# Kernel optimization log

Measured on AMD Instinct MI355X. Metric: run time of the kernel, lower is better.

Reference implementation:

```python
import jax, jax.numpy as jnp
import numpy as np

B, T = 32, 4096
I_CND2 = 512      # 2 * size_i_cnd
EMB = 256         # size_i_embed_ar
H = 896           # size_h_rnn
FC = 896          # size_h_fc
O = 512           # size_o


def setup_inputs() -> dict:
    key = jax.random.key(0)
    ks = jax.random.split(key, 8)
    s = 0.02
    return {
        "reference_sample": jax.random.randint(ks[0], (B, T), 0, O),
        "i_cnd_series": jax.random.normal(ks[1], (B, T, I_CND2), dtype=jnp.float32),
        "emb": jax.random.normal(ks[2], (O, EMB), dtype=jnp.float32) * s,
        "w_ih": jax.random.normal(ks[3], (3 * H, EMB + I_CND2), dtype=jnp.float32) * s,
        "w_hh": jax.random.normal(ks[4], (3 * H, H), dtype=jnp.float32) * s,
        "b_ih": jnp.zeros((3 * H,), jnp.float32),
        "b_hh": jnp.zeros((3 * H,), jnp.float32),
        "fc1_w": jax.random.normal(ks[5], (FC, H), dtype=jnp.float32) * s,
        "fc1_b": jnp.zeros((FC,), jnp.float32),
        "fc2_w": jax.random.normal(ks[6], (O, FC), dtype=jnp.float32) * s,
        "fc2_b": jnp.zeros((O,), jnp.float32),
    }


def _gru_scan(gates_x, w_hh, b_hh):
    # gates_x: (B, T, 3H) precomputed input projections (torch gate order: r, z, n)
    h0 = jnp.zeros((gates_x.shape[0], H), gates_x.dtype)

    def step(h, gx):
        gh = h @ w_hh.T + b_hh
        xr, xz, xn = jnp.split(gx, 3, axis=-1)
        hr, hz, hn = jnp.split(gh, 3, axis=-1)
        r = jax.nn.sigmoid(xr + hr)
        z = jax.nn.sigmoid(xz + hz)
        n = jnp.tanh(xn + r * hn)
        h_new = (1.0 - z) * n + z * h
        return h_new, h_new

    _, hs = jax.lax.scan(step, h0, jnp.swapaxes(gates_x, 0, 1))  # (T, B, H)
    return jnp.swapaxes(hs, 0, 1)  # (B, T, H)


def reference(reference_sample, i_cnd_series, emb, w_ih, w_hh, b_ih, b_hh,
              fc1_w, fc1_b, fc2_w, fc2_b):
    # embedding + concat with conditioning
    x = jnp.concatenate([emb[reference_sample], i_cnd_series], axis=-1)  # (B,T,EMB+2C)
    # batch all input-side GRU matmuls (compute-dense), scan only hidden recurrence
    gates_x = jnp.einsum('btd,gd->btg', x, w_ih) + b_ih  # (B,T,3H)
    o_rnn = _gru_scan(gates_x, w_hh, b_hh)               # (B,T,H)
    hidden = jax.nn.relu(jnp.einsum('bth,fh->btf', o_rnn, fc1_w) + fc1_b)
    return jnp.einsum('btf,of->bto', hidden, fc2_w) + fc2_b  # (B,T,O)
```

## Files before the change

kernel.cpp:

```cpp
#include <hip/hip_runtime.h>

#define B_ 32
#define T_FULL 4096
#define EMB_ 256
#define XD_ 768
#define H_ 896
#define G3_ 2688
#define O_ 512
#define NWG_SCAN 28
#define THR_SCAN 768

typedef __attribute__((ext_vector_type(8))) short bf16x8;
typedef __attribute__((ext_vector_type(4))) float f32x4;
typedef __attribute__((ext_vector_type(16))) float f32x16;

__device__ __forceinline__ f32x4 mfma16(bf16x8 a, bf16x8 b, f32x4 c) {
  return __builtin_amdgcn_mfma_f32_16x16x32_bf16(a, b, c, 0, 0, 0);
}
__device__ __forceinline__ f32x16 mfma32(bf16x8 a, bf16x8 b, f32x16 c) {
  return __builtin_amdgcn_mfma_f32_32x32x16_bf16(a, b, c, 0, 0, 0);
}

__device__ __forceinline__ unsigned short f2bf(float x) {
  union { float f; unsigned u; } v; v.f = x;
  unsigned r = v.u + 0x7fffu + ((v.u >> 16) & 1u);
  return (unsigned short)(r >> 16);
}
__device__ __forceinline__ float bf2f(unsigned short h) {
  union { float f; unsigned u; } v; v.u = ((unsigned)h) << 16;
  return v.f;
}

__device__ __forceinline__ unsigned long long aload64(const unsigned long long* p) {
  return __hip_atomic_load((unsigned long long*)p, __ATOMIC_RELAXED, __HIP_MEMORY_SCOPE_AGENT);
}
__device__ __forceinline__ unsigned aload32(const unsigned* p) {
  return __hip_atomic_load((unsigned*)p, __ATOMIC_RELAXED, __HIP_MEMORY_SCOPE_AGENT);
}
__device__ __forceinline__ void astore32(unsigned* p, unsigned v) {
  __hip_atomic_store(p, v, __ATOMIC_RELAXED, __HIP_MEMORY_SCOPE_AGENT);
}

__device__ __forceinline__ int hswz(int row, int cb) {
  const int g = cb >> 4;
  const int gs = (g & ~15) | ((g & 15) ^ (row & 15));
  return row * 1792 + (gs << 4) + (cb & 15);
}

__global__ __launch_bounds__(256) void cvt_bf16(const float* __restrict__ in,
                                                unsigned short* __restrict__ out, int n) {
  for (int i = blockIdx.x * 256 + threadIdx.x; i < n; i += gridDim.x * 256)
    out[i] = f2bf(in[i]);
}

template<int VAR>
__global__ __launch_bounds__(256) void gemm_bf16(
    const unsigned short* __restrict__ A,
    const int* __restrict__ sample,
    const float* __restrict__ icnd,
    const unsigned short* __restrict__ embb,
    const unsigned short* __restrict__ W,
    const float* __restrict__ bias,
    float* __restrict__ outf,
    unsigned short* __restrict__ outb,
    int t0) {
  constexpr int K = (VAR == 0) ? XD_ : H_;
  constexpr int N = (VAR == 0) ? G3_ : (VAR == 1 ? H_ : O_);
  constexpr int LDT = 48;
  __shared__ __align__(16) unsigned short Asl[128 * LDT];
  __shared__ __align__(16) unsigned short Bsl[128 * LDT];
  const int tid = threadIdx.x;
  const int rowBase = blockIdx.y * 128, colBase = blockIdx.x * 128;
  const int lane = tid & 63, wid = tid >> 6;
  const int wm = wid >> 1, wn = wid & 1;
  const int lr = lane & 15, lk = lane >> 4;
  const f32x4 fzero = {0.f, 0.f, 0.f, 0.f};
  f32x4 acc[4][4];
#pragma unroll
  for (int i = 0; i < 4; ++i)
#pragma unroll
    for (int j = 0; j < 4; ++j) acc[i][j] = fzero;

  for (int k0 = 0; k0 < K; k0 += 32) {
#pragma unroll
    for (int s = 0; s < 2; ++s) {
      const int seg = tid + s * 256;
      const int r = seg >> 2, kg = (seg & 3) * 8;
      const int kk = k0 + kg;
      bf16x8 va;
      if (VAR == 0) {
        const int rowG = rowBase + r;
        const int b = rowG & 31, t = t0 + (rowG >> 5);
        if (kk < EMB_) {
          const int e = sample[b * T_FULL + t];
          va = *(const bf16x8*)(embb + e * EMB_ + kk);
        } else {
          const float* p = icnd + ((size_t)(b * T_FULL + t)) * 512 + (kk - EMB_);
          const float4 f0 = *(const float4*)p;
          const float4 f1 = *(const float4*)(p + 4);
          va[0] = (short)f2bf(f0.x); va[1] = (short)f2bf(f0.y);
          va[2] = (short)f2bf(f0.z); va[3] = (short)f2bf(f0.w);
          va[4] = (short)f2bf(f1.x); va[5] = (short)f2bf(f1.y);
          va[6] = (short)f2bf(f1.z); va[7] = (short)f2bf(f1.w);
        }
      } else {
        va = *(const bf16x8*)(A + (size_t)(rowBase + r) * K + kk);
      }
      *(bf16x8*)(Asl + r * LDT + kg) = va;
      *(bf16x8*)(Bsl + r * LDT + kg) = *(const bf16x8*)(W + (size_t)(colBase + r) * K + kk);
    }
    __syncthreads();
    bf16x8 af[4], bfr[4];
#pragma unroll
    for (int mt = 0; mt < 4; ++mt)
      af[mt] = *(const bf16x8*)(Asl + (wm * 64 + mt * 16 + lr) * LDT + lk * 8);
#pragma unroll
    for (int nt = 0; nt < 4; ++nt)
      bfr[nt] = *(const bf16x8*)(Bsl + (wn * 64 + nt * 16 + lr) * LDT + lk * 8);
#pragma unroll
    for (int mt = 0; mt < 4; ++mt)
#pragma unroll
      for (int nt = 0; nt < 4; ++nt) acc[mt][nt] = mfma16(af[mt], bfr[nt], acc[mt][nt]);
    __syncthreads();
  }

#pragma unroll
  for (int mt = 0; mt < 4; ++mt) {
#pragma unroll
    for (int nt = 0; nt < 4; ++nt) {
      const int colG = colBase + wn * 64 + nt * 16 + lr;
      const float bv = bias[colG];
#pragma unroll
      for (int r = 0; r < 4; ++r) {
        const int rowG = rowBase + wm * 64 + mt * 16 + lk * 4 + r;
        const float v = acc[mt][nt][r] + bv;
        if (VAR == 0) {
          outf[(size_t)rowG * N + colG] = v;
        } else if (VAR == 1) {
          outb[(size_t)rowG * N + colG] = f2bf(fmaxf(v, 0.f));
        } else {
          const int b = rowG & 31, t = t0 + (rowG >> 5);
          outf[((size_t)(b * T_FULL + t)) * O_ + colG] = v;
        }
      }
    }
  }
}

__global__ __launch_bounds__(THR_SCAN, 3) void scan_gru(
    const float* __restrict__ gates,
    const unsigned short* __restrict__ whh,
    const float* __restrict__ bhh,
    unsigned long long* __restrict__ hbuf,
    unsigned short* __restrict__ ornn,
    unsigned int* __restrict__ arr,
    int t0, int Tc) {
  __shared__ __align__(16) char hst[114688];
  __shared__ float gh2f[2 * 96 * 32];
  const int tid = threadIdx.x;
  const int j0 = blockIdx.x * 32;
  const int lane = tid & 63, wid = tid >> 6;
  const int l31 = lane & 31, lhi = lane >> 5;
  const int eb = tid >> 4, ec = (tid & 15) * 2;

  float bh0 = 0.f, bh1 = 0.f, bh2 = 0.f, bh3 = 0.f, bh4 = 0.f, bh5 = 0.f;
  float hown0 = 0.f, hown1 = 0.f;
  if (tid < 512) {
    const int j = j0 + ec;
    bh0 = bhh[j];          bh1 = bhh[j + 1];
    bh2 = bhh[H_ + j];     bh3 = bhh[H_ + j + 1];
    bh4 = bhh[2 * H_ + j]; bh5 = bhh[2 * H_ + j + 1];
    const int rb0 = (t0 + 1) & 1;
    const char* hb = (const char*)hbuf + rb0 * 114688;
    const int off = hswz(eb, 2 * j);
    const unsigned hi01 = aload32((const unsigned*)(hb + off));
    const unsigned lo01 = aload32((const unsigned*)(hb + off + 57344));
    hown0 = bf2f((unsigned short)(hi01 & 0xffff)) + bf2f((unsigned short)(lo01 & 0xffff));
    hown1 = bf2f((unsigned short)(hi01 >> 16)) + bf2f((unsigned short)(lo01 >> 16));
  }

  for (int tl = 0; tl < Tc; ++tl) {
    const int t = t0 + tl;
    const int rb = (t + 1) & 1, wb = t & 1;

    float2 pxr = {0.f, 0.f}, pxz = {0.f, 0.f}, pxn = {0.f, 0.f};
    if (tid < 512) {
      const float* gx = gates + ((size_t)tl * 32 + eb) * G3_;
      pxr = *(const float2*)(gx + j0 + ec);
      pxz = *(const float2*)(gx + H_ + j0 + ec);
      pxn = *(const float2*)(gx + 2 * H_ + j0 + ec);
    }
    {
      const unsigned long long* src = hbuf + (size_t)rb * 14336;
      unsigned long long rg[10];
#pragma unroll
      for (int k = 0; k < 10; ++k) rg[k] = aload64(src + tid + k * 768);
      __builtin_amdgcn_sched_barrier(0);
#pragma unroll
      for (int k = 0; k < 10; ++k)
        *(unsigned long long*)(hst + (size_t)(tid + k * 768) * 8) = rg[k];
      unsigned long long rg2[9];
#pragma unroll
      for (int k = 0; k < 9; ++k) {
        const int i = tid + (10 + k) * 768;
        rg2[k] = (i < 14336) ? aload64(src + i) : 0ull;
      }
      __builtin_amdgcn_sched_barrier(0);
#pragma unroll
      for (int k = 0; k < 9; ++k) {
        const int i = tid + (10 + k) * 768;
        if (i < 14336) *(unsigned long long*)(hst + (size_t)i * 8) = rg2[k];
      }
    }
    __syncthreads();

    if (wid < 6) {
      const int s2 = wid >> 1, kh = wid & 1;
      const unsigned short* wp =
          whh + (size_t)(s2 * H_ + j0 + l31) * H_ + kh * 448 + lhi * 8;
      f32x16 acc;
#pragma unroll
      for (int r = 0; r < 16; ++r) acc[r] = 0.f;
#pragma unroll
      for (int i = 0; i < 28; ++i) {
        const int g = (kh * 28 + i) * 2 + lhi;
        const int gs = (g & ~15) | ((g & 15) ^ (l31 & 15));
        const int off = l31 * 1792 + (gs << 4);
        const bf16x8 bh = *(const bf16x8*)(hst + off);
        const bf16x8 bl = *(const bf16x8*)(hst + 57344 + off);
        const bf16x8 bw = *(const bf16x8*)(wp + i * 16);
        acc = mfma32(bw, bh, acc);
        acc = mfma32(bw, bl, acc);
      }
#pragma unroll
      for (int r = 0; r < 16; ++r) {
        const int rowD = (r & 3) + 8 * (r >> 2) + 4 * lhi;
        gh2f[(kh * 96 + s2 * 32 + rowD) * 32 + (l31 ^ rowD)] = acc[r];
      }
    }
    __syncthreads();

    if (tid < 512) {
      const int b0 = (0 * 32 + ec) * 32, b1 = (1 * 32 + ec) * 32, b2 = (2 * 32 + ec) * 32;
      const int c0 = eb ^ ec, c1 = eb ^ (ec + 1);
      const float ghr0 = gh2f[b0 + c0] + gh2f[3072 + b0 + c0] + bh0;
      const float ghr1 = gh2f[b0 + 32 + c1] + gh2f[3072 + b0 + 32 + c1] + bh1;
      const float ghz0 = gh2f[b1 + c0] + gh2f[3072 + b1 + c0] + bh2;
      const float ghz1 = gh2f[b1 + 32 + c1] + gh2f[3072 + b1 + 32 + c1] + bh3;
      const float ghn0 = gh2f[b2 + c0] + gh2f[3072 + b2 + c0] + bh4;
      const float ghn1 = gh2f[b2 + 32 + c1] + gh2f[3072 + b2 + 32 + c1] + bh5;
      const float r0 = 1.f / (1.f + __expf(-(pxr.x + ghr0)));
      const float r1 = 1.f / (1.f + __expf(-(pxr.y + ghr1)));
      const float z0 = 1.f / (1.f + __expf(-(pxz.x + ghz0)));
      const float z1 = 1.f / (1.f + __expf(-(pxz.y + ghz1)));
      const float e0 = __expf(2.f * (pxn.x + r0 * ghn0));
      const float e1 = __expf(2.f * (pxn.y + r1 * ghn1));
      const float n0 = 1.f - 2.f / (e0 + 1.f);
      const float n1 = 1.f - 2.f / (e1 + 1.f);
      hown0 = (1.f - z0) * n0 + z0 * hown0;
      hown1 = (1.f - z1) * n1 + z1 * hown1;
      const unsigned short h0 = f2bf(hown0), h1 = f2bf(hown1);
      const unsigned short l0 = f2bf(hown0 - bf2f(h0)), l1 = f2bf(hown1 - bf2f(h1));
      const unsigned hi01 = (unsigned)h0 | ((unsigned)h1 << 16);
      const unsigned lo01 = (unsigned)l0 | ((unsigned)l1 << 16);
      char* hb = (char*)hbuf + wb * 114688;
      const int off = hswz(eb, 2 * (j0 + ec));
      astore32((unsigned*)(hb + off), hi01);
      astore32((unsigned*)(hb + off + 57344), lo01);
      *(unsigned*)(ornn + ((size_t)tl * 32 + eb) * H_ + j0 + ec) = hi01;
    }

    asm volatile("s_waitcnt vmcnt(0)" ::: "memory");
    __syncthreads();
    const unsigned tgt = (unsigned)(t + 1);
    if (tid == 0) astore32(arr + blockIdx.x, tgt);
    if (wid == 0) {
      for (;;) {
        const unsigned v = (lane < NWG_SCAN) ? aload32(arr + lane) : tgt;
        if (__all(v >= tgt)) break;
        __builtin_amdgcn_s_sleep(1);
      }
    }
    __syncthreads();
  }
}

extern "C" void kernel_launch(void* const* d_in, const int* in_sizes, int n_in,
                              void* d_out, int out_size, void* d_ws, size_t ws_size,
                              hipStream_t stream) {
  (void)in_sizes; (void)n_in; (void)out_size;
  const int* sample = (const int*)d_in[0];
  const float* icnd = (const float*)d_in[1];
  const float* emb = (const float*)d_in[2];
  const float* wih = (const float*)d_in[3];
  const float* whh = (const float*)d_in[4];
  const float* bih = (const float*)d_in[5];
  const float* bhh = (const float*)d_in[6];
  const float* fc1w = (const float*)d_in[7];
  const float* fc1b = (const float*)d_in[8];
  const float* fc2w = (const float*)d_in[9];
  const float* fc2b = (const float*)d_in[10];
  float* out = (float*)d_out;
  char* ws = (char*)d_ws;

  size_t off = 0;
  auto alloc = [&](size_t bytes) {
    size_t o = off;
    off = (off + bytes + 255) & ~(size_t)255;
    return o;
  };
  const size_t o_arr = alloc(256);
  const size_t o_h = alloc((size_t)2 * 114688);
  const size_t zero_end = off;
  const size_t o_emb = alloc((size_t)O_ * EMB_ * 2);
  const size_t o_wih = alloc((size_t)G3_ * XD_ * 2);
  const size_t o_whh = alloc((size_t)G3_ * H_ * 2);
  const size_t o_f1w = alloc((size_t)H_ * H_ * 2);
  const size_t o_f2w = alloc((size_t)O_ * H_ * 2);
  const size_t head = off;

  int Tc = 512;
  while (Tc > 8) {
    size_t need = head + (size_t)Tc * 32 * G3_ * 4 + 2 * ((size_t)Tc * 32 * H_ * 2) + 4096;
    if (need <= ws_size) break;
    Tc >>= 1;
  }
  const size_t o_gat = alloc((size_t)Tc * 32 * G3_ * 4);
  const size_t o_orn = alloc((size_t)Tc * 32 * H_ * 2);
  const size_t o_hid = alloc((size_t)Tc * 32 * H_ * 2);
  (void)o_gat; (void)o_orn; (void)o_hid;

  unsigned short* embb = (unsigned short*)(ws + o_emb);
  unsigned short* wihb = (unsigned short*)(ws + o_wih);
  unsigned short* whhb = (unsigned short*)(ws + o_whh);
  unsigned short* f1wb = (unsigned short*)(ws + o_f1w);
  unsigned short* f2wb = (unsigned short*)(ws + o_f2w);
  float* gat = (float*)(ws + o_gat);
  unsigned short* orn = (unsigned short*)(ws + o_orn);
  unsigned short* hid = (unsigned short*)(ws + o_hid);
  unsigned long long* hbuf = (unsigned long long*)(ws + o_h);
  unsigned int* arr = (unsigned int*)(ws + o_arr);

  (void)hipMemsetAsync(ws, 0, zero_end, stream);

  cvt_bf16<<<512, 256, 0, stream>>>(emb, embb, O_ * EMB_);
  cvt_bf16<<<1024, 256, 0, stream>>>(wih, wihb, G3_ * XD_);
  cvt_bf16<<<1024, 256, 0, stream>>>(whh, whhb, G3_ * H_);
  cvt_bf16<<<512, 256, 0, stream>>>(fc1w, f1wb, H_ * H_);
  cvt_bf16<<<512, 256, 0, stream>>>(fc2w, f2wb, O_ * H_);

  const int nch = T_FULL / Tc;
  const int M = Tc * 32;
  for (int c = 0; c < nch; ++c) {
    const int t0 = c * Tc;
    gemm_bf16<0><<<dim3(G3_ / 128, M / 128), 256, 0, stream>>>(
        nullptr, sample, icnd, embb, wihb, bih, gat, nullptr, t0);
    scan_gru<<<NWG_SCAN, THR_SCAN, 0, stream>>>(gat, whhb, bhh, hbuf, orn, arr, t0, Tc);
    gemm_bf16<1><<<dim3(H_ / 128, M / 128), 256, 0, stream>>>(
        orn, nullptr, nullptr, nullptr, f1wb, fc1b, nullptr, hid, t0);
    gemm_bf16<2><<<dim3(O_ / 128, M / 128), 256, 0, stream>>>(
        hid, nullptr, nullptr, nullptr, f2wb, fc2b, out, nullptr, t0);
  }
}
```

Measured before the change: 39.67 ms.

## Replace GRU scan grid barrier with per-block flags and blocked hidden layout

```diff
diff --git a/kernel.cpp b/kernel.cpp
--- a/kernel.cpp
+++ b/kernel.cpp
@@ -39,12 +39,6 @@
 }
 __device__ __forceinline__ void astore32(unsigned* p, unsigned v) {
   __hip_atomic_store(p, v, __ATOMIC_RELAXED, __HIP_MEMORY_SCOPE_AGENT);
-}
-
-__device__ __forceinline__ int hswz(int row, int cb) {
-  const int g = cb >> 4;
-  const int gs = (g & ~15) | ((g & 15) ^ (row & 15));
-  return row * 1792 + (gs << 4) + (cb & 15);
 }
 
 __global__ __launch_bounds__(256) void cvt_bf16(const float* __restrict__ in,
@@ -153,12 +147,13 @@
     const float* __restrict__ bhh,
     unsigned long long* __restrict__ hbuf,
     unsigned short* __restrict__ ornn,
-    unsigned int* __restrict__ arr,
+    unsigned int* __restrict__ flags,
     int t0, int Tc) {
   __shared__ __align__(16) char hst[114688];
   __shared__ float gh2f[2 * 96 * 32];
   const int tid = threadIdx.x;
-  const int j0 = blockIdx.x * 32;
+  const int jbo = blockIdx.x;
+  const int j0 = jbo * 32;
   const int lane = tid & 63, wid = tid >> 6;
   const int l31 = lane & 31, lhi = lane >> 5;
   const int eb = tid >> 4, ec = (tid & 15) * 2;
@@ -172,9 +167,9 @@
     bh4 = bhh[2 * H_ + j]; bh5 = bhh[2 * H_ + j + 1];
     const int rb0 = (t0 + 1) & 1;
     const char* hb = (const char*)hbuf + rb0 * 114688;
-    const int off = hswz(eb, 2 * j);
-    const unsigned hi01 = aload32((const unsigned*)(hb + off));
-    const unsigned lo01 = aload32((const unsigned*)(hb + off + 57344));
+    const int o = jbo * 2048 + eb * 64 + ec * 2;
+    const unsigned hi01 = aload32((const unsigned*)(hb + o));
+    const unsigned lo01 = aload32((const unsigned*)(hb + o + 57344));
     hown0 = bf2f((unsigned short)(hi01 & 0xffff)) + bf2f((unsigned short)(lo01 & 0xffff));
     hown1 = bf2f((unsigned short)(hi01 >> 16)) + bf2f((unsigned short)(lo01 >> 16));
   }
@@ -190,26 +185,29 @@
       pxz = *(const float2*)(gx + H_ + j0 + ec);
       pxn = *(const float2*)(gx + 2 * H_ + j0 + ec);
     }
+
     {
-      const unsigned long long* src = hbuf + (size_t)rb * 14336;
-      unsigned long long rg[10];
-#pragma unroll
-      for (int k = 0; k < 10; ++k) rg[k] = aload64(src + tid + k * 768);
-      __builtin_amdgcn_sched_barrier(0);
-#pragma unroll
-      for (int k = 0; k < 10; ++k)
-        *(unsigned long long*)(hst + (size_t)(tid + k * 768) * 8) = rg[k];
-      unsigned long long rg2[9];
-#pragma unroll
-      for (int k = 0; k < 9; ++k) {
-        const int i = tid + (10 + k) * 768;
-        rg2[k] = (i < 14336) ? aload64(src + i) : 0ull;
-      }
-      __builtin_amdgcn_sched_barrier(0);
-#pragma unroll
-      for (int k = 0; k < 9; ++k) {
-        const int i = tid + (10 + k) * 768;
-        if (i < 14336) *(unsigned long long*)(hst + (size_t)i * 8) = rg2[k];
+      const char* slot = (const char*)hbuf + (size_t)rb * 114688 + lhi * 57344;
+      char* dstp = hst + lhi * 57344;
+      for (int jb = wid; jb < NWG_SCAN; jb += 12) {
+        const unsigned* fl = flags + rb * 32 + jb;
+        for (;;) {
+          const unsigned v = aload32(fl);
+          if (v >= (unsigned)t) break;
+          __builtin_amdgcn_s_sleep(1);
+        }
+        const char* src = slot + jb * 2048 + l31 * 64;
+        unsigned long long rg[8];
+#pragma unroll
+        for (int q = 0; q < 8; ++q)
+          rg[q] = aload64((const unsigned long long*)(src + q * 8));
+        __builtin_amdgcn_sched_barrier(0);
+#pragma unroll
+        for (int q = 0; q < 8; ++q) {
+          const int g = jb * 4 + (q >> 1);
+          const int gs = (g & ~15) | ((g & 15) ^ (l31 & 15));
+          *(unsigned long long*)(dstp + l31 * 1792 + (gs << 4) + (q & 1) * 8) = rg[q];
+        }
       }
     }
     __syncthreads();
@@ -263,25 +261,16 @@
       const unsigned short l0 = f2bf(hown0 - bf2f(h0)), l1 = f2bf(hown1 - bf2f(h1));
       const unsigned hi01 = (unsigned)h0 | ((unsigned)h1 << 16);
       const unsigned lo01 = (unsigned)l0 | ((unsigned)l1 << 16);
-      char* hb = (char*)hbuf + wb * 114688;
-      const int off = hswz(eb, 2 * (j0 + ec));
-      astore32((unsigned*)(hb + off), hi01);
-      astore32((unsigned*)(hb + off + 57344), lo01);
+      char* hb = (char*)hbuf + (size_t)wb * 114688;
+      const int o = jbo * 2048 + eb * 64 + ec * 2;
+      astore32((unsigned*)(hb + o), hi01);
+      astore32((unsigned*)(hb + o + 57344), lo01);
       *(unsigned*)(ornn + ((size_t)tl * 32 + eb) * H_ + j0 + ec) = hi01;
     }
 
     asm volatile("s_waitcnt vmcnt(0)" ::: "memory");
     __syncthreads();
-    const unsigned tgt = (unsigned)(t + 1);
-    if (tid == 0) astore32(arr + blockIdx.x, tgt);
-    if (wid == 0) {
-      for (;;) {
-        const unsigned v = (lane < NWG_SCAN) ? aload32(arr + lane) : tgt;
-        if (__all(v >= tgt)) break;
-        __builtin_amdgcn_s_sleep(1);
-      }
-    }
-    __syncthreads();
+    if (tid == 0) astore32(flags + wb * 32 + jbo, (unsigned)(t + 1));
   }
 }
 
@@ -309,7 +298,7 @@
     off = (off + bytes + 255) & ~(size_t)255;
     return o;
   };
-  const size_t o_arr = alloc(256);
+  const size_t o_flg = alloc(256);
   const size_t o_h = alloc((size_t)2 * 114688);
   const size_t zero_end = off;
   const size_t o_emb = alloc((size_t)O_ * EMB_ * 2);
@@ -339,7 +328,7 @@
   unsigned short* orn = (unsigned short*)(ws + o_orn);
   unsigned short* hid = (unsigned short*)(ws + o_hid);
   unsigned long long* hbuf = (unsigned long long*)(ws + o_h);
-  unsigned int* arr = (unsigned int*)(ws + o_arr);
+  unsigned int* flg = (unsigned int*)(ws + o_flg);
 
   (void)hipMemsetAsync(ws, 0, zero_end, stream);
 
@@ -355,7 +344,7 @@
     const int t0 = c * Tc;
     gemm_bf16<0><<<dim3(G3_ / 128, M / 128), 256, 0, stream>>>(
         nullptr, sample, icnd, embb, wihb, bih, gat, nullptr, t0);
-    scan_gru<<<NWG_SCAN, THR_SCAN, 0, stream>>>(gat, whhb, bhh, hbuf, orn, arr, t0, Tc);
+    scan_gru<<<NWG_SCAN, THR_SCAN, 0, stream>>>(gat, whhb, bhh, hbuf, orn, flg, t0, Tc);
     gemm_bf16<1><<<dim3(H_ / 128, M / 128), 256, 0, stream>>>(
         orn, nullptr, nullptr, nullptr, f1wb, fc1b, nullptr, hid, t0);
     gemm_bf16<2><<<dim3(O_ / 128, M / 128), 256, 0, stream>>>(
```

Measured after the change: 49.79 ms. 25.5% more time.

## Halve scan workgroups, each owning 64 hidden units with full-K MFMA

Applied to the files above, without the earlier changes.

```diff
diff --git a/kernel.cpp b/kernel.cpp
--- a/kernel.cpp
+++ b/kernel.cpp
@@ -7,7 +7,7 @@
 #define H_ 896
 #define G3_ 2688
 #define O_ 512
-#define NWG_SCAN 28
+#define NWG_SCAN 14
 #define THR_SCAN 768
 
 typedef __attribute__((ext_vector_type(8))) short bf16x8;
@@ -38,6 +38,9 @@
   return __hip_atomic_load((unsigned*)p, __ATOMIC_RELAXED, __HIP_MEMORY_SCOPE_AGENT);
 }
 __device__ __forceinline__ void astore32(unsigned* p, unsigned v) {
+  __hip_atomic_store(p, v, __ATOMIC_RELAXED, __HIP_MEMORY_SCOPE_AGENT);
+}
+__device__ __forceinline__ void astore64(unsigned long long* p, unsigned long long v) {
   __hip_atomic_store(p, v, __ATOMIC_RELAXED, __HIP_MEMORY_SCOPE_AGENT);
 }
 
@@ -156,39 +159,46 @@
     unsigned int* __restrict__ arr,
     int t0, int Tc) {
   __shared__ __align__(16) char hst[114688];
-  __shared__ float gh2f[2 * 96 * 32];
+  __shared__ float gh2f[192 * 32];
   const int tid = threadIdx.x;
-  const int j0 = blockIdx.x * 32;
+  const int j0 = blockIdx.x * 64;
   const int lane = tid & 63, wid = tid >> 6;
   const int l31 = lane & 31, lhi = lane >> 5;
-  const int eb = tid >> 4, ec = (tid & 15) * 2;
-
-  float bh0 = 0.f, bh1 = 0.f, bh2 = 0.f, bh3 = 0.f, bh4 = 0.f, bh5 = 0.f;
-  float hown0 = 0.f, hown1 = 0.f;
+  const int eb = tid >> 4, ec = (tid & 15) * 4;
+
+  float bhr[4], bhz[4], bhn[4], hown[4];
+#pragma unroll
+  for (int e = 0; e < 4; ++e) { bhr[e] = 0.f; bhz[e] = 0.f; bhn[e] = 0.f; hown[e] = 0.f; }
   if (tid < 512) {
     const int j = j0 + ec;
-    bh0 = bhh[j];          bh1 = bhh[j + 1];
-    bh2 = bhh[H_ + j];     bh3 = bhh[H_ + j + 1];
-    bh4 = bhh[2 * H_ + j]; bh5 = bhh[2 * H_ + j + 1];
+    const float4 br = *(const float4*)(bhh + j);
+    const float4 bz = *(const float4*)(bhh + H_ + j);
+    const float4 bn = *(const float4*)(bhh + 2 * H_ + j);
+    bhr[0] = br.x; bhr[1] = br.y; bhr[2] = br.z; bhr[3] = br.w;
+    bhz[0] = bz.x; bhz[1] = bz.y; bhz[2] = bz.z; bhz[3] = bz.w;
+    bhn[0] = bn.x; bhn[1] = bn.y; bhn[2] = bn.z; bhn[3] = bn.w;
     const int rb0 = (t0 + 1) & 1;
     const char* hb = (const char*)hbuf + rb0 * 114688;
     const int off = hswz(eb, 2 * j);
-    const unsigned hi01 = aload32((const unsigned*)(hb + off));
-    const unsigned lo01 = aload32((const unsigned*)(hb + off + 57344));
-    hown0 = bf2f((unsigned short)(hi01 & 0xffff)) + bf2f((unsigned short)(lo01 & 0xffff));
-    hown1 = bf2f((unsigned short)(hi01 >> 16)) + bf2f((unsigned short)(lo01 >> 16));
+    const unsigned long long hi4 = aload64((const unsigned long long*)(hb + off));
+    const unsigned long long lo4 = aload64((const unsigned long long*)(hb + off + 57344));
+#pragma unroll
+    for (int e = 0; e < 4; ++e) {
+      hown[e] = bf2f((unsigned short)((hi4 >> (16 * e)) & 0xffff)) +
+                bf2f((unsigned short)((lo4 >> (16 * e)) & 0xffff));
+    }
   }
 
   for (int tl = 0; tl < Tc; ++tl) {
     const int t = t0 + tl;
     const int rb = (t + 1) & 1, wb = t & 1;
 
-    float2 pxr = {0.f, 0.f}, pxz = {0.f, 0.f}, pxn = {0.f, 0.f};
+    float4 pxr = {0.f, 0.f, 0.f, 0.f}, pxz = {0.f, 0.f, 0.f, 0.f}, pxn = {0.f, 0.f, 0.f, 0.f};
     if (tid < 512) {
       const float* gx = gates + ((size_t)tl * 32 + eb) * G3_;
-      pxr = *(const float2*)(gx + j0 + ec);
-      pxz = *(const float2*)(gx + H_ + j0 + ec);
-      pxn = *(const float2*)(gx + 2 * H_ + j0 + ec);
+      pxr = *(const float4*)(gx + j0 + ec);
+      pxz = *(const float4*)(gx + H_ + j0 + ec);
+      pxn = *(const float4*)(gx + 2 * H_ + j0 + ec);
     }
     {
       const unsigned long long* src = hbuf + (size_t)rb * 14336;
@@ -215,15 +225,15 @@
     __syncthreads();
 
     if (wid < 6) {
-      const int s2 = wid >> 1, kh = wid & 1;
+      const int s2 = wid >> 1, ut = wid & 1;
       const unsigned short* wp =
-          whh + (size_t)(s2 * H_ + j0 + l31) * H_ + kh * 448 + lhi * 8;
+          whh + (size_t)(s2 * H_ + j0 + ut * 32 + l31) * H_ + lhi * 8;
       f32x16 acc;
 #pragma unroll
       for (int r = 0; r < 16; ++r) acc[r] = 0.f;
 #pragma unroll
-      for (int i = 0; i < 28; ++i) {
-        const int g = (kh * 28 + i) * 2 + lhi;
+      for (int i = 0; i < 56; ++i) {
+        const int g = i * 2 + lhi;
         const int gs = (g & ~15) | ((g & 15) ^ (l31 & 15));
         const int off = l31 * 1792 + (gs << 4);
         const bf16x8 bh = *(const bf16x8*)(hst + off);
@@ -235,39 +245,39 @@
 #pragma unroll
       for (int r = 0; r < 16; ++r) {
         const int rowD = (r & 3) + 8 * (r >> 2) + 4 * lhi;
-        gh2f[(kh * 96 + s2 * 32 + rowD) * 32 + (l31 ^ rowD)] = acc[r];
+        gh2f[(s2 * 64 + ut * 32 + rowD) * 32 + (l31 ^ rowD)] = acc[r];
       }
     }
     __syncthreads();
 
     if (tid < 512) {
-      const int b0 = (0 * 32 + ec) * 32, b1 = (1 * 32 + ec) * 32, b2 = (2 * 32 + ec) * 32;
-      const int c0 = eb ^ ec, c1 = eb ^ (ec + 1);
-      const float ghr0 = gh2f[b0 + c0] + gh2f[3072 + b0 + c0] + bh0;
-      const float ghr1 = gh2f[b0 + 32 + c1] + gh2f[3072 + b0 + 32 + c1] + bh1;
-      const float ghz0 = gh2f[b1 + c0] + gh2f[3072 + b1 + c0] + bh2;
-      const float ghz1 = gh2f[b1 + 32 + c1] + gh2f[3072 + b1 + 32 + c1] + bh3;
-      const float ghn0 = gh2f[b2 + c0] + gh2f[3072 + b2 + c0] + bh4;
-      const float ghn1 = gh2f[b2 + 32 + c1] + gh2f[3072 + b2 + 32 + c1] + bh5;
-      const float r0 = 1.f / (1.f + __expf(-(pxr.x + ghr0)));
-      const float r1 = 1.f / (1.f + __expf(-(pxr.y + ghr1)));
-      const float z0 = 1.f / (1.f + __expf(-(pxz.x + ghz0)));
-      const float z1 = 1.f / (1.f + __expf(-(pxz.y + ghz1)));
-      const float e0 = __expf(2.f * (pxn.x + r0 * ghn0));
-      const float e1 = __expf(2.f * (pxn.y + r1 * ghn1));
-      const float n0 = 1.f - 2.f / (e0 + 1.f);
-      const float n1 = 1.f - 2.f / (e1 + 1.f);
-      hown0 = (1.f - z0) * n0 + z0 * hown0;
-      hown1 = (1.f - z1) * n1 + z1 * hown1;
-      const unsigned short h0 = f2bf(hown0), h1 = f2bf(hown1);
-      const unsigned short l0 = f2bf(hown0 - bf2f(h0)), l1 = f2bf(hown1 - bf2f(h1));
-      const unsigned hi01 = (unsigned)h0 | ((unsigned)h1 << 16);
-      const unsigned lo01 = (unsigned)l0 | ((unsigned)l1 << 16);
+      unsigned long long hi4 = 0, lo4 = 0;
+      const float px_r[4] = {pxr.x, pxr.y, pxr.z, pxr.w};
+      const float px_z[4] = {pxz.x, pxz.y, pxz.z, pxz.w};
+      const float px_n[4] = {pxn.x, pxn.y, pxn.z, pxn.w};
+#pragma unroll
+      for (int e = 0; e < 4; ++e) {
+        const int uu = ec + e;
+        const int col = eb ^ (uu & 31);
+        const float ghr = gh2f[uu * 32 + col] + bhr[e];
+        const float ghz = gh2f[(64 + uu) * 32 + col] + bhz[e];
+        const float ghn = gh2f[(128 + uu) * 32 + col] + bhn[e];
+        const float r0 = 1.f / (1.f + __expf(-(px_r[e] + ghr)));
+        const float z0 = 1.f / (1.f + __expf(-(px_z[e] + ghz)));
+        const float e0 = __expf(2.f * (px_n[e] + r0 * ghn));
+        const float n0 = 1.f - 2.f / (e0 + 1.f);
+        const float hnew = (1.f - z0) * n0 + z0 * hown[e];
+        hown[e] = hnew;
+        const unsigned short h0 = f2bf(hnew);
+        const unsigned short l0 = f2bf(hnew - bf2f(h0));
+        hi4 |= ((unsigned long long)h0) << (16 * e);
+        lo4 |= ((unsigned long long)l0) << (16 * e);
+      }
       char* hb = (char*)hbuf + wb * 114688;
       const int off = hswz(eb, 2 * (j0 + ec));
-      astore32((unsigned*)(hb + off), hi01);
-      astore32((unsigned*)(hb + off + 57344), lo01);
-      *(unsigned*)(ornn + ((size_t)tl * 32 + eb) * H_ + j0 + ec) = hi01;
+      astore64((unsigned long long*)(hb + off), hi4);
+      astore64((unsigned long long*)(hb + off + 57344), lo4);
+      *(unsigned long long*)(ornn + ((size_t)tl * 32 + eb) * H_ + j0 + ec) = hi4;
     }
 
     asm volatile("s_waitcnt vmcnt(0)" ::: "memory");
@@ -278,7 +288,6 @@
       for (;;) {
         const unsigned v = (lane < NWG_SCAN) ? aload32(arr + lane) : tgt;
         if (__all(v >= tgt)) break;
-        __builtin_amdgcn_s_sleep(1);
       }
     }
     __syncthreads();
```

Measured after the change: 60.05 ms. 1.51x slower.
